# Kernel tuning notes

Measured on AMD Instinct MI355X. Metric: run time of the kernel, lower is better.

Reference implementation:

```python
import jax, jax.numpy as jnp
import numpy as np

THETA = 10000.0
NUM_HEADS = 16


def _rope(x, pos, theta):
    # x: [..., T, d_k], pos: [T]
    d_k = x.shape[-1]
    inv_freq = 1.0 / theta ** (jnp.arange(0, d_k, 2, dtype=jnp.float32) / d_k)
    ang = pos.astype(jnp.float32)[:, None] * inv_freq  # [T, d_k/2]
    cos, sin = jnp.cos(ang), jnp.sin(ang)
    x1, x2 = x[..., ::2], x[..., 1::2]
    even = x1 * cos - x2 * sin
    odd = x1 * sin + x2 * cos
    return jnp.stack([even, odd], axis=-1).reshape(x.shape)


def setup_inputs() -> dict:
    key = jax.random.key(0)
    ks = jax.random.split(key, 5)
    B, T, D = 4, 2048, 1024
    return {
        "in_features": jax.random.normal(ks[0], (B, T, D), dtype=jnp.float32),
        "token_positions": jnp.arange(T, dtype=jnp.int64 if jax.config.jax_enable_x64 else jnp.int32),
        "Wq": jax.random.normal(ks[1], (D, D), dtype=jnp.float32) * 0.02,
        "Wk": jax.random.normal(ks[2], (D, D), dtype=jnp.float32) * 0.02,
        "Wv": jax.random.normal(ks[3], (D, D), dtype=jnp.float32) * 0.02,
        "Wo": jax.random.normal(ks[4], (D, D), dtype=jnp.float32) * 0.02,
    }


def reference(in_features, token_positions, Wq, Wk, Wv, Wo):
    B, T, D = in_features.shape
    h = NUM_HEADS
    d_k = D // h
    # projections (weight stored [out, in], torch applies x @ W.T)
    Q = in_features @ Wq.T
    K = in_features @ Wk.T
    V = in_features @ Wv.T
    # [B, T, h*d_k] -> [B, h, T, d_k]
    Q = Q.reshape(B, T, h, d_k).transpose(0, 2, 1, 3)
    K = K.reshape(B, T, h, d_k).transpose(0, 2, 1, 3)
    V = V.reshape(B, T, h, d_k).transpose(0, 2, 1, 3)
    Q = _rope(Q, token_positions, THETA)
    K = _rope(K, token_positions, THETA)
    scores = jnp.einsum("bhqd,bhkd->bhqk", Q, K) / jnp.sqrt(jnp.float32(d_k))
    causal = jnp.tril(jnp.ones((T, T), dtype=bool))
    scores = jnp.where(causal, scores, -jnp.inf)
    attn = jax.nn.softmax(scores, axis=-1)
    heads = jnp.einsum("bhqk,bhkd->bhqd", attn, V)
    out = heads.transpose(0, 2, 1, 3).reshape(B, T, D)
    return out @ Wo.T
```

## Files before the change

### kernel.cpp

```cpp
#include <hip/hip_runtime.h>


typedef unsigned short u16;
typedef short short8 __attribute__((ext_vector_type(8)));
typedef float f32x4 __attribute__((ext_vector_type(4)));

#if defined(__has_builtin)
#if __has_builtin(__builtin_amdgcn_exp2f)
#define EXP2(x) __builtin_amdgcn_exp2f(x)
#else
#define EXP2(x) exp2f(x)
#endif
#else
#define EXP2(x) exp2f(x)
#endif

#define QSCALE 0.18033688011112042f

__device__ __forceinline__ float bf2f(u16 u) {
  return __uint_as_float(((unsigned int)u) << 16);
}
__device__ __forceinline__ u16 f2bf(float f) {
  unsigned int x = __float_as_uint(f);
  x += 0x7fff + ((x >> 16) & 1);
  return (u16)(x >> 16);
}

__device__ __forceinline__ void glds16(const u16* g, u16* l) {
  __builtin_amdgcn_global_load_lds(
      (const __attribute__((address_space(1))) unsigned int*)g,
      (__attribute__((address_space(3))) unsigned int*)l, 16, 0, 0);
}

__global__ __launch_bounds__(256) void cvt_bf16(const float* __restrict__ in,
                                                u16* __restrict__ out) {
  const int i = (blockIdx.x * 256 + threadIdx.x) * 8;
  const float4 a = *(const float4*)(in + i);
  const float4 b = *(const float4*)(in + i + 4);
  short8 o;
  o[0] = (short)f2bf(a.x); o[1] = (short)f2bf(a.y);
  o[2] = (short)f2bf(a.z); o[3] = (short)f2bf(a.w);
  o[4] = (short)f2bf(b.x); o[5] = (short)f2bf(b.y);
  o[6] = (short)f2bf(b.z); o[7] = (short)f2bf(b.w);
  *(short8*)(out + i) = o;
}

__global__ __launch_bounds__(256) void gemm_qkv(const u16* __restrict__ A,
                                                const u16* __restrict__ W,
                                                const float2* __restrict__ tab,
                                                u16* __restrict__ Qr,
                                                u16* __restrict__ Kr,
                                                u16* __restrict__ Vd) {
  const int K = 1024;
  __shared__ __align__(16) u16 As[128 * 32];
  __shared__ __align__(16) u16 Bs[128 * 32];
  const int tid = threadIdx.x;
  const int m0 = blockIdx.y << 7;
  const int n0 = blockIdx.x << 7;
  const int w = tid >> 6, L = tid & 63;
  const int wm = (w >> 1) << 6, wn = (w & 1) << 6;
  const int lane15 = L & 15, quad = L >> 4;
  const int koff = quad << 3;

  f32x4 acc[4][4] = {};

  const int s0 = tid, s1 = tid + 256;
  const int r0 = s0 >> 2, c0 = (s0 & 3) << 3;
  const int r1 = s1 >> 2, c1 = (s1 & 3) << 3;
  const u16* A0 = A + (size_t)(m0 + r0) * K + c0;
  const u16* A1 = A + (size_t)(m0 + r1) * K + c1;
  const u16* B0 = W + (size_t)(n0 + r0) * K + c0;
  const u16* B1 = W + (size_t)(n0 + r1) * K + c1;
  u16* asd0 = &As[s0 * 8]; u16* asd1 = &As[s1 * 8];
  u16* bsd0 = &Bs[s0 * 8]; u16* bsd1 = &Bs[s1 * 8];

  for (int k0 = 0; k0 < K; k0 += 32) {
    __syncthreads();
    glds16(A0 + k0, asd0);
    glds16(A1 + k0, asd1);
    glds16(B0 + k0, bsd0);
    glds16(B1 + k0, bsd1);
    __syncthreads();
    short8 a[4], b[4];
#pragma unroll
    for (int mt = 0; mt < 4; ++mt)
      a[mt] = *(const short8*)&As[(wm + mt * 16 + lane15) * 32 + koff];
#pragma unroll
    for (int nt = 0; nt < 4; ++nt)
      b[nt] = *(const short8*)&Bs[(wn + nt * 16 + lane15) * 32 + koff];
#pragma unroll
    for (int mt = 0; mt < 4; ++mt)
#pragma unroll
      for (int nt = 0; nt < 4; ++nt)
        acc[mt][nt] =
            __builtin_amdgcn_mfma_f32_16x16x32_bf16(a[mt], b[nt], acc[mt][nt], 0, 0, 0);
  }

  const int sel = n0 >> 10;
  const int ncol0 = (n0 & 1023) + wn;
  if (sel == 2) {
#pragma unroll
    for (int mt = 0; mt < 4; ++mt) {
      const int rbase = m0 + wm + mt * 16 + (quad << 2);
#pragma unroll
      for (int nt = 0; nt < 4; ++nt) {
        const int col = ncol0 + nt * 16 + lane15;
#pragma unroll
        for (int r = 0; r < 4; ++r)
          Vd[(size_t)(rbase + r) * 1024 + col] = f2bf(acc[mt][nt][r]);
      }
    }
  } else {
    u16* dst = sel ? Kr : Qr;
    const float sc = sel ? 1.0f : QSCALE;
#pragma unroll
    for (int mt = 0; mt < 4; ++mt) {
      const int rbase = m0 + wm + mt * 16 + (quad << 2);
#pragma unroll
      for (int nt = 0; nt < 4; ++nt) {
        const int col = ncol0 + nt * 16 + lane15;
        const int h = col >> 6, dcol = col & 63, d2 = dcol >> 1;
#pragma unroll
        for (int r = 0; r < 4; ++r) {
          const int m = rbase + r;
          const int bb = m >> 11, tt = m & 2047;
          const float2 cs = tab[(tt << 5) + d2];
          const float self = acc[mt][nt][r];
          const float part = __shfl_xor(self, 1, 64);
          const float res = (dcol & 1) ? (part * cs.y + self * cs.x)
                                       : (self * cs.x - part * cs.y);
          dst[(((size_t)((bb * 16 + h) * 2048 + tt)) << 6) + dcol] = f2bf(res * sc);
        }
      }
    }
  }
}

__global__ __launch_bounds__(256) void gemm_bt(const u16* __restrict__ A,
                                               const u16* __restrict__ B,
                                               float* __restrict__ C,
                                               int M, int N, int K) {
  __shared__ __align__(16) u16 As[128 * 32];
  __shared__ __align__(16) u16 Bs[128 * 32];
  const int tid = threadIdx.x;
  const int m0 = blockIdx.y << 7;
  const int n0 = blockIdx.x << 7;
  const int w = tid >> 6, L = tid & 63;
  const int wm = (w >> 1) << 6, wn = (w & 1) << 6;
  const int lane15 = L & 15, quad = L >> 4;
  const int koff = quad << 3;

  f32x4 acc[4][4] = {};

  const int s0 = tid, s1 = tid + 256;
  const int r0 = s0 >> 2, c0 = (s0 & 3) << 3;
  const int r1 = s1 >> 2, c1 = (s1 & 3) << 3;
  const u16* A0 = A + (size_t)(m0 + r0) * K + c0;
  const u16* A1 = A + (size_t)(m0 + r1) * K + c1;
  const u16* B0 = B + (size_t)(n0 + r0) * K + c0;
  const u16* B1 = B + (size_t)(n0 + r1) * K + c1;
  u16* asd0 = &As[s0 * 8]; u16* asd1 = &As[s1 * 8];
  u16* bsd0 = &Bs[s0 * 8]; u16* bsd1 = &Bs[s1 * 8];

  for (int k0 = 0; k0 < K; k0 += 32) {
    __syncthreads();
    glds16(A0 + k0, asd0);
    glds16(A1 + k0, asd1);
    glds16(B0 + k0, bsd0);
    glds16(B1 + k0, bsd1);
    __syncthreads();
    short8 a[4], b[4];
#pragma unroll
    for (int mt = 0; mt < 4; ++mt)
      a[mt] = *(const short8*)&As[(wm + mt * 16 + lane15) * 32 + koff];
#pragma unroll
    for (int nt = 0; nt < 4; ++nt)
      b[nt] = *(const short8*)&Bs[(wn + nt * 16 + lane15) * 32 + koff];
#pragma unroll
    for (int mt = 0; mt < 4; ++mt)
#pragma unroll
      for (int nt = 0; nt < 4; ++nt)
        acc[mt][nt] =
            __builtin_amdgcn_mfma_f32_16x16x32_bf16(a[mt], b[nt], acc[mt][nt], 0, 0, 0);
  }

#pragma unroll
  for (int mt = 0; mt < 4; ++mt) {
    const int rbase = m0 + wm + mt * 16 + (quad << 2);
#pragma unroll
    for (int nt = 0; nt < 4; ++nt) {
      const int col = n0 + wn + nt * 16 + lane15;
#pragma unroll
      for (int r = 0; r < 4; ++r)
        C[(size_t)(rbase + r) * N + col] = acc[mt][nt][r];
    }
  }
}

__global__ __launch_bounds__(256) void rope_table(const int* __restrict__ pos,
                                                  float2* __restrict__ tab) {
  const int gid = blockIdx.x * 256 + threadIdx.x;
  const int d2 = gid & 31;
  const int t = gid >> 5;
  double inv = pow(10000.0, -(double)d2 / 32.0);
  double ang = (double)pos[t] * inv;
  tab[gid] = make_float2((float)cos(ang), (float)sin(ang));
}

__global__ __launch_bounds__(256) void transpose_v(const u16* __restrict__ Vlin,
                                                   u16* __restrict__ Vt) {
  __shared__ __align__(16) u16 tile[64][68];
  const int tid = threadIdx.x;
  const int bh = blockIdx.y, b = bh >> 4, h = bh & 15;
  const int t0 = blockIdx.x << 6;
#pragma unroll
  for (int i = 0; i < 4; ++i) {
    int s = tid + (i << 8);
    int tl = s >> 4, c4 = (s & 15) << 2;
    *(uint2*)&tile[tl][c4] =
        *(const uint2*)(Vlin + (((size_t)(b * 2048 + t0 + tl)) << 10) + (h << 6) + c4);
  }
  __syncthreads();
#pragma unroll
  for (int i = 0; i < 4; ++i) {
    int s = tid + (i << 8);
    int d = s >> 4, t4 = (s & 15) << 2;
    uint2 o;
    o.x = (unsigned)tile[t4 + 0][d] | ((unsigned)tile[t4 + 1][d] << 16);
    o.y = (unsigned)tile[t4 + 2][d] | ((unsigned)tile[t4 + 3][d] << 16);
    *(uint2*)(Vt + (((size_t)(bh * 64 + d)) << 11) + t0 + t4) = o;
  }
}

__global__ __launch_bounds__(256) void flash_attn(const u16* __restrict__ Q,
                                                  const u16* __restrict__ Kk,
                                                  const u16* __restrict__ Vt,
                                                  u16* __restrict__ O) {
  __shared__ __align__(16) u16 Ksm[64 * 72];
  __shared__ __align__(16) u16 Vsm[64 * 72];
  __shared__ __align__(16) u16 Psm[8][16 * 64];
  const int tid = threadIdx.x;
  const int w = tid >> 6, L = tid & 63;
  const int lane15 = L & 15, quad = L >> 4;
  const int qt = 15 - (blockIdx.x >> 6);
  const int bh = blockIdx.x & 63;
  const int b = bh >> 4, h = bh & 15;
  const int rq = lane15 >> 2;
  const int nkt = 2 * qt + 2;

  const int s0 = tid, s1 = tid + 256;
  const u16* kbase = Kk + ((size_t)bh << 17);
  const u16* kp0 = kbase + s0 * 8;
  const u16* kp1 = kbase + s1 * 8;
  const u16* vbase = Vt + ((size_t)bh << 17);
  const u16* vp0 = vbase + (size_t)(s0 >> 3) * 2048 + (s0 & 7) * 8;
  const u16* vp1 = vbase + (size_t)(s1 >> 3) * 2048 + (s1 & 7) * 8;
  const int d0 = (s0 >> 3) * 72 + (s0 & 7) * 8;
  const int d1 = (s1 >> 3) * 72 + (s1 & 7) * 8;

  const size_t qrow = (size_t)bh * 2048 + qt * 128 + w * 32;
  short8 qa[2][2];
#pragma unroll
  for (int hf = 0; hf < 2; ++hf) {
    const size_t qb = (qrow + hf * 16 + lane15) << 6;
    qa[hf][0] = *(const short8*)(Q + qb + (quad << 3));
    qa[hf][1] = *(const short8*)(Q + qb + 32 + (quad << 3));
  }

  uint4 kr0 = *(const uint4*)kp0;
  uint4 kr1 = *(const uint4*)kp1;
  uint4 vr0 = *(const uint4*)vp0;
  uint4 vr1 = *(const uint4*)vp1;
  *(uint4*)&Ksm[d0] = kr0; *(uint4*)&Ksm[d1] = kr1;
  *(uint4*)&Vsm[d0] = vr0; *(uint4*)&Vsm[d1] = vr1;
  __syncthreads();

  f32x4 o_acc[2][4] = {};
  float l_part[2][4] = {};

  for (int kt = 0; kt < nkt; ++kt) {
    if (kt + 1 < nkt) {
      kr0 = *(const uint4*)(kp0 + (size_t)(kt + 1) * 4096);
      kr1 = *(const uint4*)(kp1 + (size_t)(kt + 1) * 4096);
      vr0 = *(const uint4*)(vp0 + (kt + 1) * 64);
      vr1 = *(const uint4*)(vp1 + (kt + 1) * 64);
    }

    short8 kb[4][2];
#pragma unroll
    for (int nt = 0; nt < 4; ++nt) {
      kb[nt][0] = *(const short8*)&Ksm[(nt * 16 + lane15) * 72 + (quad << 3)];
      kb[nt][1] = *(const short8*)&Ksm[(nt * 16 + lane15) * 72 + 32 + (quad << 3)];
    }

#pragma unroll
    for (int hf = 0; hf < 2; ++hf) {
      const int B0 = qt * 128 + w * 32 + hf * 16;
      if (kt * 64 > B0 + 15) continue;
      u16* pw = Psm[w * 2 + hf];

      f32x4 sc[4];
#pragma unroll
      for (int nt = 0; nt < 4; ++nt) {
        f32x4 a = {};
        a = __builtin_amdgcn_mfma_f32_16x16x32_bf16(qa[hf][0], kb[nt][0], a, 0, 0, 0);
        a = __builtin_amdgcn_mfma_f32_16x16x32_bf16(qa[hf][1], kb[nt][1], a, 0, 0, 0);
        sc[nt] = a;
      }

      if (kt * 64 + 63 > B0) {
#pragma unroll
        for (int nt = 0; nt < 4; ++nt)
#pragma unroll
          for (int r = 0; r < 4; ++r) {
            const int row = B0 + (quad << 2) + r;
            const int key = kt * 64 + nt * 16 + lane15;
            if (key > row) sc[nt][r] = -1e30f;
          }
      }

      asm volatile("" ::: "memory");
#pragma unroll
      for (int nt = 0; nt < 4; ++nt) {
        const int colsw = ((nt ^ quad) << 4) + lane15;
#pragma unroll
        for (int r = 0; r < 4; ++r) {
          const float p = EXP2(sc[nt][r]);
          l_part[hf][r] += p;
          pw[((quad << 2) + r) * 64 + colsw] = (u16)(__float_as_uint(p) >> 16);
        }
      }
      asm volatile("" ::: "memory");

#pragma unroll
      for (int ks = 0; ks < 2; ++ks) {
        const short8 pa =
            *(const short8*)&pw[lane15 * 64 + ((ks * 32 + quad * 8) ^ (rq << 4))];
#pragma unroll
        for (int dt = 0; dt < 4; ++dt) {
          const short8 vb =
              *(const short8*)&Vsm[(dt * 16 + lane15) * 72 + ks * 32 + quad * 8];
          o_acc[hf][dt] =
              __builtin_amdgcn_mfma_f32_16x16x32_bf16(pa, vb, o_acc[hf][dt], 0, 0, 0);
        }
      }
    }

    if (kt + 1 < nkt) {
      __syncthreads();
      *(uint4*)&Ksm[d0] = kr0; *(uint4*)&Ksm[d1] = kr1;
      *(uint4*)&Vsm[d0] = vr0; *(uint4*)&Vsm[d1] = vr1;
      __syncthreads();
    }
  }

#pragma unroll
  for (int hf = 0; hf < 2; ++hf) {
#pragma unroll
    for (int r = 0; r < 4; ++r) {
      float l = l_part[hf][r];
#pragma unroll
      for (int off = 1; off < 16; off <<= 1) l += __shfl_xor(l, off, 64);
      const float inv = 1.f / l;
      const int t = qt * 128 + w * 32 + hf * 16 + (quad << 2) + r;
      const size_t obase = (((size_t)b * 2048 + t) << 10) + (h << 6);
#pragma unroll
      for (int dt = 0; dt < 4; ++dt)
        O[obase + dt * 16 + lane15] = f2bf(o_acc[hf][dt][r] * inv);
    }
  }
}

extern "C" void kernel_launch(void* const* d_in, const int* in_sizes, int n_in,
                              void* d_out, int out_size, void* d_ws, size_t ws_size,
                              hipStream_t stream) {
  const float* X  = (const float*)d_in[0];
  const int* pos  = (const int*)d_in[1];
  const float* Wq = (const float*)d_in[2];
  const float* Wk = (const float*)d_in[3];
  const float* Wv = (const float*)d_in[4];
  const float* Wo = (const float*)d_in[5];
  float* out = (float*)d_out;

  char* ws = (char*)d_ws;
  const size_t SZ = (size_t)8192 * 1024 * sizeof(u16);
  const size_t WSZ = (size_t)1024 * 1024 * sizeof(u16);
  u16* Vlin = (u16*)(ws + 0 * SZ);
  u16* Qr   = (u16*)(ws + 1 * SZ);
  u16* Kr   = (u16*)(ws + 2 * SZ);
  u16* Vt   = (u16*)(ws + 3 * SZ);
  u16* Xb   = (u16*)(ws + 4 * SZ);
  u16* Oh   = Vlin;
  char* wtail = ws + 5 * SZ;
  u16* Wqkvb = (u16*)(wtail);
  u16* Wob   = (u16*)(wtail + 3 * WSZ);
  float2* tab = (float2*)(wtail + 4 * WSZ);

  const dim3 blk(256);

  cvt_bf16<<<4096, blk, 0, stream>>>(X, Xb);
  cvt_bf16<<<512, blk, 0, stream>>>(Wq, Wqkvb);
  cvt_bf16<<<512, blk, 0, stream>>>(Wk, Wqkvb + 1024 * 1024);
  cvt_bf16<<<512, blk, 0, stream>>>(Wv, Wqkvb + 2 * 1024 * 1024);
  cvt_bf16<<<512, blk, 0, stream>>>(Wo, Wob);
  rope_table<<<256, blk, 0, stream>>>(pos, tab);
  gemm_qkv<<<dim3(24, 64), blk, 0, stream>>>(Xb, Wqkvb, tab, Qr, Kr, Vlin);
  transpose_v<<<dim3(32, 64), blk, 0, stream>>>(Vlin, Vt);
  flash_attn<<<1024, blk, 0, stream>>>(Qr, Kr, Vt, Oh);
  gemm_bt<<<dim3(8, 64), blk, 0, stream>>>(Oh, Wob, out, 8192, 1024, 1024);
}
```

Baseline: 296.4 us.

## Compute RoPE sin/cos inline in QKV epilogue and shrink output GEMM tile

Removes the separate RoPE table kernel and computes the inverse frequencies and sin/cos directly in the QKV GEMM epilogue with fast intrinsics. This avoids a launch and the table memory reads. It also halves the M tile of the output projection GEMM to 64 rows, doubling the block count for better CU occupancy and load balance. The fast sincos intrinsic on large angles may reduce accuracy, and the smaller tile lowers data reuse per block.

New measurement: 292.8 us. No clear change (-1.2%).

```diff
diff --git a/kernel.cpp b/kernel.cpp
--- a/kernel.cpp
+++ b/kernel.cpp
@@ -16,6 +16,7 @@
 #endif
 
 #define QSCALE 0.18033688011112042f
+#define NEG_L2T_32 -0.4152410118609203f
 
 __device__ __forceinline__ float bf2f(u16 u) {
   return __uint_as_float(((unsigned int)u) << 16);
@@ -47,7 +48,7 @@
 
 __global__ __launch_bounds__(256) void gemm_qkv(const u16* __restrict__ A,
                                                 const u16* __restrict__ W,
-                                                const float2* __restrict__ tab,
+                                                const int* __restrict__ pos,
                                                 u16* __restrict__ Qr,
                                                 u16* __restrict__ Kr,
                                                 u16* __restrict__ Vd) {
@@ -113,22 +114,30 @@
   } else {
     u16* dst = sel ? Kr : Qr;
     const float sc = sel ? 1.0f : QSCALE;
+    float invf[4];
+#pragma unroll
+    for (int nt = 0; nt < 4; ++nt) {
+      const int d2 = ((ncol0 + nt * 16 + lane15) & 63) >> 1;
+      invf[nt] = EXP2((float)d2 * NEG_L2T_32);
+    }
 #pragma unroll
     for (int mt = 0; mt < 4; ++mt) {
       const int rbase = m0 + wm + mt * 16 + (quad << 2);
 #pragma unroll
-      for (int nt = 0; nt < 4; ++nt) {
-        const int col = ncol0 + nt * 16 + lane15;
-        const int h = col >> 6, dcol = col & 63, d2 = dcol >> 1;
-#pragma unroll
-        for (int r = 0; r < 4; ++r) {
-          const int m = rbase + r;
-          const int bb = m >> 11, tt = m & 2047;
-          const float2 cs = tab[(tt << 5) + d2];
+      for (int r = 0; r < 4; ++r) {
+        const int m = rbase + r;
+        const int bb = m >> 11, tt = m & 2047;
+        const float posf = (float)pos[tt];
+#pragma unroll
+        for (int nt = 0; nt < 4; ++nt) {
+          const int col = ncol0 + nt * 16 + lane15;
+          const int h = col >> 6, dcol = col & 63;
+          float sn, cn;
+          __sincosf(posf * invf[nt], &sn, &cn);
           const float self = acc[mt][nt][r];
           const float part = __shfl_xor(self, 1, 64);
-          const float res = (dcol & 1) ? (part * cs.y + self * cs.x)
-                                       : (self * cs.x - part * cs.y);
+          const float res = (dcol & 1) ? (part * sn + self * cn)
+                                       : (self * cn - part * sn);
           dst[(((size_t)((bb * 16 + h) * 2048 + tt)) << 6) + dcol] = f2bf(res * sc);
         }
       }
@@ -140,44 +149,40 @@
                                                const u16* __restrict__ B,
                                                float* __restrict__ C,
                                                int M, int N, int K) {
-  __shared__ __align__(16) u16 As[128 * 32];
+  __shared__ __align__(16) u16 As[64 * 32];
   __shared__ __align__(16) u16 Bs[128 * 32];
   const int tid = threadIdx.x;
-  const int m0 = blockIdx.y << 7;
+  const int m0 = blockIdx.y << 6;
   const int n0 = blockIdx.x << 7;
   const int w = tid >> 6, L = tid & 63;
-  const int wm = (w >> 1) << 6, wn = (w & 1) << 6;
+  const int wm = (w >> 1) << 5, wn = (w & 1) << 6;
   const int lane15 = L & 15, quad = L >> 4;
   const int koff = quad << 3;
 
-  f32x4 acc[4][4] = {};
+  f32x4 acc[2][4] = {};
 
   const int s0 = tid, s1 = tid + 256;
-  const int r0 = s0 >> 2, c0 = (s0 & 3) << 3;
-  const int r1 = s1 >> 2, c1 = (s1 & 3) << 3;
-  const u16* A0 = A + (size_t)(m0 + r0) * K + c0;
-  const u16* A1 = A + (size_t)(m0 + r1) * K + c1;
-  const u16* B0 = B + (size_t)(n0 + r0) * K + c0;
-  const u16* B1 = B + (size_t)(n0 + r1) * K + c1;
-  u16* asd0 = &As[s0 * 8]; u16* asd1 = &As[s1 * 8];
+  const u16* A0 = A + (size_t)(m0 + (s0 >> 2)) * K + ((s0 & 3) << 3);
+  const u16* B0 = B + (size_t)(n0 + (s0 >> 2)) * K + ((s0 & 3) << 3);
+  const u16* B1 = B + (size_t)(n0 + (s1 >> 2)) * K + ((s1 & 3) << 3);
+  u16* asd0 = &As[s0 * 8];
   u16* bsd0 = &Bs[s0 * 8]; u16* bsd1 = &Bs[s1 * 8];
 
   for (int k0 = 0; k0 < K; k0 += 32) {
     __syncthreads();
     glds16(A0 + k0, asd0);
-    glds16(A1 + k0, asd1);
     glds16(B0 + k0, bsd0);
     glds16(B1 + k0, bsd1);
     __syncthreads();
-    short8 a[4], b[4];
-#pragma unroll
-    for (int mt = 0; mt < 4; ++mt)
+    short8 a[2], b[4];
+#pragma unroll
+    for (int mt = 0; mt < 2; ++mt)
       a[mt] = *(const short8*)&As[(wm + mt * 16 + lane15) * 32 + koff];
 #pragma unroll
     for (int nt = 0; nt < 4; ++nt)
       b[nt] = *(const short8*)&Bs[(wn + nt * 16 + lane15) * 32 + koff];
 #pragma unroll
-    for (int mt = 0; mt < 4; ++mt)
+    for (int mt = 0; mt < 2; ++mt)
 #pragma unroll
       for (int nt = 0; nt < 4; ++nt)
         acc[mt][nt] =
@@ -185,7 +190,7 @@
   }
 
 #pragma unroll
-  for (int mt = 0; mt < 4; ++mt) {
+  for (int mt = 0; mt < 2; ++mt) {
     const int rbase = m0 + wm + mt * 16 + (quad << 2);
 #pragma unroll
     for (int nt = 0; nt < 4; ++nt) {
@@ -195,16 +200,6 @@
         C[(size_t)(rbase + r) * N + col] = acc[mt][nt][r];
     }
   }
-}
-
-__global__ __launch_bounds__(256) void rope_table(const int* __restrict__ pos,
-                                                  float2* __restrict__ tab) {
-  const int gid = blockIdx.x * 256 + threadIdx.x;
-  const int d2 = gid & 31;
-  const int t = gid >> 5;
-  double inv = pow(10000.0, -(double)d2 / 32.0);
-  double ang = (double)pos[t] * inv;
-  tab[gid] = make_float2((float)cos(ang), (float)sin(ang));
 }
 
 __global__ __launch_bounds__(256) void transpose_v(const u16* __restrict__ Vlin,
@@ -394,7 +389,6 @@
   char* wtail = ws + 5 * SZ;
   u16* Wqkvb = (u16*)(wtail);
   u16* Wob   = (u16*)(wtail + 3 * WSZ);
-  float2* tab = (float2*)(wtail + 4 * WSZ);
 
   const dim3 blk(256);
 
@@ -403,9 +397,8 @@
   cvt_bf16<<<512, blk, 0, stream>>>(Wk, Wqkvb + 1024 * 1024);
   cvt_bf16<<<512, blk, 0, stream>>>(Wv, Wqkvb + 2 * 1024 * 1024);
   cvt_bf16<<<512, blk, 0, stream>>>(Wo, Wob);
-  rope_table<<<256, blk, 0, stream>>>(pos, tab);
-  gemm_qkv<<<dim3(24, 64), blk, 0, stream>>>(Xb, Wqkvb, tab, Qr, Kr, Vlin);
+  gemm_qkv<<<dim3(24, 64), blk, 0, stream>>>(Xb, Wqkvb, pos, Qr, Kr, Vlin);
   transpose_v<<<dim3(32, 64), blk, 0, stream>>>(Vlin, Vt);
   flash_attn<<<1024, blk, 0, stream>>>(Qr, Kr, Vt, Oh);
-  gemm_bt<<<dim3(8, 64), blk, 0, stream>>>(Oh, Wob, out, 8192, 1024, 1024);
-}
+  gemm_bt<<<dim3(8, 128), blk, 0, stream>>>(Oh, Wob, out, 8192, 1024, 1024);
+}
```
